# Kernel tuning notes

Hardware: AMD Instinct MI355X
Metric: run time of the kernel (lower is better)

The kernel has to match this reference:

```python
import jax, jax.numpy as jnp
import numpy as np

GRID_SIZE = 5


def kan_layer(x, spline_weight, spline_scaler, grid):
    # x: (B, In); spline_weight: (Out, In, G); spline_scaler: (Out, In); grid: (G,)
    xn = jnp.tanh(x)                                   # (B, In)
    # distances: (B, Out, In, G) via broadcast of (B,1,In,1) against (G,)
    distances = jnp.abs(xn[:, None, :, None] - grid)
    weights = jnp.exp(-distances * spline_scaler[None, :, :, None])
    # double sum over grid then in_features, fused into one einsum
    return jnp.einsum('boig,oig->bo', weights, spline_weight)


def setup_inputs() -> dict:
    key = jax.random.key(0)
    ks = jax.random.split(key, 7)
    B, D_IN, D_H, D_OUT = 2048, 128, 256, 64
    return {
        'x':  jax.random.normal(ks[0], (B, D_IN), dtype=jnp.float32),
        'w1': jax.random.normal(ks[1], (D_H, D_IN, GRID_SIZE), dtype=jnp.float32),
        's1': jax.random.normal(ks[2], (D_H, D_IN), dtype=jnp.float32),
        'w2': jax.random.normal(ks[3], (D_H // 2, D_H, GRID_SIZE), dtype=jnp.float32),
        's2': jax.random.normal(ks[4], (D_H // 2, D_H), dtype=jnp.float32),
        'w3': jax.random.normal(ks[5], (D_OUT, D_H // 2, GRID_SIZE), dtype=jnp.float32),
        's3': jax.random.normal(ks[6], (D_OUT, D_H // 2), dtype=jnp.float32),
    }


def reference(x, w1, s1, w2, s2, w3, s3):
    grid = jnp.linspace(-1.0, 1.0, GRID_SIZE, dtype=jnp.float32)  # registered buffer
    h1 = jax.nn.relu(kan_layer(x, w1, s1, grid))
    h2 = jax.nn.relu(kan_layer(h1, w2, s2, grid))
    out = jax.nn.sigmoid(kan_layer(h2, w3, s3, grid))
    return out
```

## Files before the change

kernel.cpp:

```cpp
#include <hip/hip_runtime.h>
#include <math.h>

#define GRID_N 5
#define LOG2E 1.4426950408889634f

__global__ void prep_tab(const float* __restrict__ w, const float* __restrict__ s,
                         float* __restrict__ T, float* __restrict__ Kt, int O, int I) {
    int idx = blockIdx.x * 256 + threadIdx.x;
    if (idx >= O * I) return;
    int o = idx / I, i = idx % I;
    float K = -s[idx] * LOG2E;
    const float gv[5] = {-1.f, -0.5f, 0.f, 0.5f, 1.f};
    float A[6], B[6];
    A[0] = 0.f; B[5] = 0.f;
#pragma unroll
    for (int g = 0; g < 5; g++) {
        float wv = w[idx * GRID_N + g];
        A[g + 1] = A[g] + wv * __builtin_amdgcn_exp2f(-K * gv[g]);
    }
#pragma unroll
    for (int g = 4; g >= 0; g--) {
        float wv = w[idx * GRID_N + g];
        B[g] = B[g + 1] + wv * __builtin_amdgcn_exp2f(K * gv[g]);
    }
#pragma unroll
    for (int k = 0; k < 6; k++) {
        T[((i * 6 + k) * O + o) * 2 + 0] = A[k];
        T[((i * 6 + k) * O + o) * 2 + 1] = B[k];
    }
    Kt[i * O + o] = K;
}

template<int IN, int OUT, int ACT, int BT, int NT>
__global__ __launch_bounds__(NT) void kan_layer(
    const float* __restrict__ x,
    const float* __restrict__ T,
    const float* __restrict__ Kt,
    float* __restrict__ out)
{
    constexpr int WB  = NT / OUT;
    constexpr int BPT = BT / WB;
    __shared__ float xn[BT][IN];
    __shared__ int   bn[BT][IN];

    const int tid = threadIdx.x;
    const int b0  = blockIdx.x * BT;

    for (int e = tid; e < BT * IN; e += NT) {
        int bb = e / IN, ii = e % IN;
        float v  = x[(b0 + bb) * IN + ii];
        float ex = __builtin_amdgcn_exp2f(2.0f * LOG2E * v);
        float xv = 1.0f - 2.0f / (ex + 1.0f);
        int k = (int)((xv + 1.0f) * 2.0f) + 1;
        k = k > 5 ? 5 : k;
        xn[bb][ii] = xv;
        bn[bb][ii] = k * (OUT * 2);
    }
    __syncthreads();

    const int o  = tid % OUT;
    const int bg = tid / OUT;
    const float* To = T + o * 2;

    float acc[BPT];
#pragma unroll
    for (int j = 0; j < BPT; j++) acc[j] = 0.f;

#pragma unroll 4
    for (int i = 0; i < IN; i++) {
        float K   = Kt[i * OUT + o];
        int  base = i * (6 * OUT * 2);
#pragma unroll
        for (int j = 0; j < BPT; j++) {
            float xv  = xn[bg * BPT + j][i];
            int   off = bn[bg * BPT + j][i];
            float2 ab = *reinterpret_cast<const float2*>(To + base + off);
            float t = K * xv;
            acc[j] += ab.x * __builtin_amdgcn_exp2f(t)
                    + ab.y * __builtin_amdgcn_exp2f(-t);
        }
    }

#pragma unroll
    for (int j = 0; j < BPT; j++) {
        int b = b0 + bg * BPT + j;
        float z = acc[j];
        if (ACT == 0) {
            z = fmaxf(z, 0.f);
        } else {
            float e2 = __builtin_amdgcn_exp2f(-LOG2E * z);
            z = 1.0f / (1.0f + e2);
        }
        out[b * OUT + o] = z;
    }
}

extern "C" void kernel_launch(void* const* d_in, const int* in_sizes, int n_in,
                              void* d_out, int out_size, void* d_ws, size_t ws_size,
                              hipStream_t stream) {
    const float* x  = (const float*)d_in[0];
    const float* w1 = (const float*)d_in[1];
    const float* s1 = (const float*)d_in[2];
    const float* w2 = (const float*)d_in[3];
    const float* s2 = (const float*)d_in[4];
    const float* w3 = (const float*)d_in[5];
    const float* s3 = (const float*)d_in[6];
    float* out = (float*)d_out;

    float* ws  = (float*)d_ws;
    float* h1  = ws;
    float* h2  = h1  + 524288;
    float* T1  = h2  + 262144;
    float* K1  = T1  + 393216;
    float* T2  = K1  + 32768;
    float* K2  = T2  + 393216;
    float* T3  = K2  + 32768;
    float* K3  = T3  + 98304;

    prep_tab<<<128, 256, 0, stream>>>(w1, s1, T1, K1, 256, 128);
    prep_tab<<<128, 256, 0, stream>>>(w2, s2, T2, K2, 128, 256);
    prep_tab<<< 32, 256, 0, stream>>>(w3, s3, T3, K3,  64, 128);

    kan_layer<128, 256, 0, 2, 256><<<1024, 256, 0, stream>>>(x,  T1, K1, h1);
    kan_layer<256, 128, 0, 4, 256><<< 512, 256, 0, stream>>>(h1, T2, K2, h2);
    kan_layer<128,  64, 1, 4, 256><<< 512, 256, 0, stream>>>(h2, T3, K3, out);
}
```

Baseline: 111.5 us.

## Replace shared-memory input staging with per-wave register readlane broadcast

Each wave now loads its batch rows directly into registers, computes tanh and the grid bin per lane, and broadcasts them across the wave with readlane instead of staging them through shared memory behind a block barrier. The work split also changes to one wave per 64 outputs by a small batch group, with fewer batch rows per thread for layers 2 and 3. This removes the LDS traffic and the synchronisation. The cost is less reuse of each K and table load across batch rows, plus more register pressure.

```diff
diff --git a/kernel.cpp b/kernel.cpp
--- a/kernel.cpp
+++ b/kernel.cpp
@@ -3,6 +3,7 @@
 
 #define GRID_N 5
 #define LOG2E 1.4426950408889634f
+#define EXP2F __builtin_amdgcn_exp2f
 
 __global__ void prep_tab(const float* __restrict__ w, const float* __restrict__ s,
                          float* __restrict__ T, float* __restrict__ Kt, int O, int I) {
@@ -16,12 +17,12 @@
 #pragma unroll
     for (int g = 0; g < 5; g++) {
         float wv = w[idx * GRID_N + g];
-        A[g + 1] = A[g] + wv * __builtin_amdgcn_exp2f(-K * gv[g]);
+        A[g + 1] = A[g] + wv * EXP2F(-K * gv[g]);
     }
 #pragma unroll
     for (int g = 4; g >= 0; g--) {
         float wv = w[idx * GRID_N + g];
-        B[g] = B[g + 1] + wv * __builtin_amdgcn_exp2f(K * gv[g]);
+        B[g] = B[g + 1] + wv * EXP2F(K * gv[g]);
     }
 #pragma unroll
     for (int k = 0; k < 6; k++) {
@@ -31,67 +32,70 @@
     Kt[i * O + o] = K;
 }
 
-template<int IN, int OUT, int ACT, int BT, int NT>
-__global__ __launch_bounds__(NT) void kan_layer(
-    const float* __restrict__ x,
+template<int IN, int OUT, int ACT, int BPT>
+__global__ __launch_bounds__(256) void kan_layer(
+    const float* __restrict__ xin,
     const float* __restrict__ T,
     const float* __restrict__ Kt,
     float* __restrict__ out)
 {
-    constexpr int WB  = NT / OUT;
-    constexpr int BPT = BT / WB;
-    __shared__ float xn[BT][IN];
-    __shared__ int   bn[BT][IN];
+    constexpr int OCH = OUT / 64;
+    constexpr int CH  = IN / 64;
+    const int lane = threadIdx.x & 63;
+    const int wid  = (blockIdx.x << 2) | (threadIdx.x >> 6);
+    const int oc   = wid % OCH;
+    const int bg   = wid / OCH;
+    const int o    = (oc << 6) | lane;
+    const int b0   = bg * BPT;
 
-    const int tid = threadIdx.x;
-    const int b0  = blockIdx.x * BT;
-
-    for (int e = tid; e < BT * IN; e += NT) {
-        int bb = e / IN, ii = e % IN;
-        float v  = x[(b0 + bb) * IN + ii];
-        float ex = __builtin_amdgcn_exp2f(2.0f * LOG2E * v);
-        float xv = 1.0f - 2.0f / (ex + 1.0f);
-        int k = (int)((xv + 1.0f) * 2.0f) + 1;
-        k = k > 5 ? 5 : k;
-        xn[bb][ii] = xv;
-        bn[bb][ii] = k * (OUT * 2);
-    }
-    __syncthreads();
-
-    const int o  = tid % OUT;
-    const int bg = tid / OUT;
-    const float* To = T + o * 2;
+    float xv[BPT][CH];
+    int   bo[BPT][CH];
+#pragma unroll
+    for (int j = 0; j < BPT; j++)
+#pragma unroll
+        for (int c = 0; c < CH; c++) {
+            float v  = xin[(b0 + j) * IN + (c << 6) + lane];
+            float ex = EXP2F(2.0f * LOG2E * v);
+            float t  = 1.0f - 2.0f / (ex + 1.0f);
+            xv[j][c] = t;
+            int k = (int)((t + 1.0f) * 2.0f) + 1;
+            bo[j][c] = (k > 5 ? 5 : k) * (OUT * 8);
+        }
 
     float acc[BPT];
 #pragma unroll
     for (int j = 0; j < BPT; j++) acc[j] = 0.f;
 
-#pragma unroll 4
-    for (int i = 0; i < IN; i++) {
-        float K   = Kt[i * OUT + o];
-        int  base = i * (6 * OUT * 2);
+    const char*  Tb = (const char*)T;
+    const float* Kp = Kt + o;
+
 #pragma unroll
-        for (int j = 0; j < BPT; j++) {
-            float xv  = xn[bg * BPT + j][i];
-            int   off = bn[bg * BPT + j][i];
-            float2 ab = *reinterpret_cast<const float2*>(To + base + off);
-            float t = K * xv;
-            acc[j] += ab.x * __builtin_amdgcn_exp2f(t)
-                    + ab.y * __builtin_amdgcn_exp2f(-t);
+    for (int c = 0; c < CH; c++) {
+#pragma unroll 8
+        for (int l = 0; l < 64; l++) {
+            const int i = (c << 6) + l;
+            float K = Kp[i * OUT];
+            const char* Ti = Tb + (size_t)i * (6 * OUT * 8) + (o << 3);
+#pragma unroll
+            for (int j = 0; j < BPT; j++) {
+                float xs = __int_as_float(__builtin_amdgcn_readlane(__float_as_int(xv[j][c]), l));
+                int   bs = __builtin_amdgcn_readlane(bo[j][c], l);
+                const float2 ab = *(const float2*)(Ti + bs);
+                float t = K * xs;
+                acc[j] += ab.x * EXP2F(t) + ab.y * EXP2F(-t);
+            }
         }
     }
 
 #pragma unroll
     for (int j = 0; j < BPT; j++) {
-        int b = b0 + bg * BPT + j;
         float z = acc[j];
         if (ACT == 0) {
             z = fmaxf(z, 0.f);
         } else {
-            float e2 = __builtin_amdgcn_exp2f(-LOG2E * z);
-            z = 1.0f / (1.0f + e2);
+            z = 1.0f / (1.0f + EXP2F(-LOG2E * z));
         }
-        out[b * OUT + o] = z;
+        out[(b0 + j) * OUT + o] = z;
     }
 }
 
@@ -121,7 +125,7 @@
     prep_tab<<<128, 256, 0, stream>>>(w2, s2, T2, K2, 128, 256);
     prep_tab<<< 32, 256, 0, stream>>>(w3, s3, T3, K3,  64, 128);
 
-    kan_layer<128, 256, 0, 2, 256><<<1024, 256, 0, stream>>>(x,  T1, K1, h1);
-    kan_layer<256, 128, 0, 4, 256><<< 512, 256, 0, stream>>>(h1, T2, K2, h2);
-    kan_layer<128,  64, 1, 4, 256><<< 512, 256, 0, stream>>>(h2, T3, K3, out);
+    kan_layer<128, 256, 0, 2><<<1024, 256, 0, stream>>>(x,  T1, K1, h1);
+    kan_layer<256, 128, 0, 1><<<1024, 256, 0, stream>>>(h1, T2, K2, h2);
+    kan_layer<128,  64, 1, 1><<< 512, 256, 0, stream>>>(h2, T3, K3, out);
 }
```

Result: no change. 109.7 us (-1.6%).
